# Optimization experiments

Measured on AMD Instinct MI355X. Metric: run time of the kernel, lower is better.

The kernel has to match this reference:

```python
import jax, jax.numpy as jnp
import numpy as np

N_NODES = 50000
N_EDGES = 1600000
E_DIM = 128
N_LAYERS = 3
N_GRAPHS = 32


def setup_inputs() -> dict:
    key = jax.random.key(0)
    ks = jax.random.split(key, 12)
    x = jax.random.normal(ks[0], (N_NODES,), dtype=jnp.float32)
    edge_index = jax.random.randint(ks[1], (2, N_EDGES), 0, N_NODES, dtype=jnp.int32)
    batch = jnp.sort(jax.random.randint(ks[2], (N_NODES,), 0, N_GRAPHS, dtype=jnp.int32))
    s_in = 1.0  # fan_in = 1 for the first linear
    s_e = 1.0 / np.sqrt(E_DIM)
    lin_w = jax.random.normal(ks[3], (1, E_DIM), jnp.float32) * s_in
    lin_b = jax.random.normal(ks[4], (E_DIM,), jnp.float32) * 0.01
    gcn_w = jax.random.normal(ks[5], (N_LAYERS, E_DIM, E_DIM), jnp.float32) * s_e
    gcn_b = jax.random.normal(ks[6], (N_LAYERS, E_DIM), jnp.float32) * 0.01
    r1_w = jax.random.normal(ks[7], (E_DIM, E_DIM), jnp.float32) * s_e
    r1_b = jax.random.normal(ks[8], (E_DIM,), jnp.float32) * 0.01
    r2_w = jax.random.normal(ks[9], (E_DIM, 1), jnp.float32) * s_e
    r2_b = jax.random.normal(ks[10], (1,), jnp.float32) * 0.01
    return {"x": x, "edge_index": edge_index, "batch": batch,
            "lin_w": lin_w, "lin_b": lin_b, "gcn_w": gcn_w, "gcn_b": gcn_b,
            "r1_w": r1_w, "r1_b": r1_b, "r2_w": r2_w, "r2_b": r2_b}


def reference(x, edge_index, batch, lin_w, lin_b, gcn_w, gcn_b, r1_w, r1_b, r2_w, r2_b):
    # input embedding: x.view(-1, 1) @ W + b -> [N, E]
    h = x.reshape(-1, 1) @ lin_w + lin_b

    # GCN normalization (add self-loops, symmetric deg^-1/2 norm) — structure is
    # identical across layers, so compute once.
    loops = jnp.arange(N_NODES, dtype=edge_index.dtype)
    src = jnp.concatenate([edge_index[0], loops])
    dst = jnp.concatenate([edge_index[1], loops])
    deg = jax.ops.segment_sum(jnp.ones(src.shape[0], h.dtype), dst, num_segments=N_NODES)
    dinv = jnp.where(deg > 0, jax.lax.rsqrt(deg), 0.0)
    norm = (dinv[src] * dinv[dst])[:, None]  # [E+N, 1]

    # NOTE: original calls x.relu() without assignment -> no activation (faithful).
    for l in range(N_LAYERS):
        h = h @ gcn_w[l]                                        # [N, E]
        h = jax.ops.segment_sum(h[src] * norm, dst, num_segments=N_NODES) + gcn_b[l]

    # global_add_pool over graphs
    pooled = jax.ops.segment_sum(h, batch, num_segments=N_GRAPHS)  # [G, E]
    hr = jnp.tanh(pooled @ r1_w + r1_b)
    return hr @ r2_w + r2_b  # [G, 1]
```

## Files before the change

### kernel.cpp

```cpp
#include <hip/hip_runtime.h>
#include <math.h>

#define NGRAPH 32
#define CAP 10240
#define EPT 16
#define EPB (256 * EPT)
#define BLK 256

__device__ __forceinline__ int block_scan_excl(int v, int tid, int* wsum, int& total) {
    int x = v;
#pragma unroll
    for (int d = 1; d < 64; d <<= 1) {
        int t = __shfl_up(x, d);
        if ((tid & 63) >= d) x += t;
    }
    if ((tid & 63) == 63) wsum[tid >> 6] = x;
    __syncthreads();
    if (tid == 0) {
        int a = 0;
#pragma unroll
        for (int i = 0; i < 4; i++) { int t = wsum[i]; wsum[i] = a; a += t; }
        wsum[4] = a;
    }
    __syncthreads();
    total = wsum[4];
    return x - v + wsum[tid >> 6];
}

__global__ __launch_bounds__(256, 4) void k_part(
        const int* __restrict__ src, const int* __restrict__ dst,
        int* __restrict__ gcursor, unsigned int* __restrict__ packed, int E) {
    __shared__ unsigned int ldsbuf[EPB];
    __shared__ int hist[256], lofs[256], lcur[256], base[256], wsum[5];
    int tid = threadIdx.x;
    int e0 = blockIdx.x * EPB;
    hist[tid] = 0;
    __syncthreads();
    int d_[EPT], s_[EPT];
#pragma unroll
    for (int c = 0; c < EPT / 4; c++) {
        int e = e0 + c * 1024 + (tid << 2);
        if (e + 3 < E) {
            int4 dv = *(const int4*)&dst[e];
            int4 sv = *(const int4*)&src[e];
            d_[4*c+0] = dv.x; d_[4*c+1] = dv.y; d_[4*c+2] = dv.z; d_[4*c+3] = dv.w;
            s_[4*c+0] = sv.x; s_[4*c+1] = sv.y; s_[4*c+2] = sv.z; s_[4*c+3] = sv.w;
            atomicAdd(&hist[dv.x >> 8], 1);
            atomicAdd(&hist[dv.y >> 8], 1);
            atomicAdd(&hist[dv.z >> 8], 1);
            atomicAdd(&hist[dv.w >> 8], 1);
        } else {
#pragma unroll
            for (int k = 0; k < 4; k++) {
                int ee = e + k;
                if (ee < E) {
                    d_[4*c+k] = dst[ee]; s_[4*c+k] = src[ee];
                    atomicAdd(&hist[d_[4*c+k] >> 8], 1);
                } else {
                    d_[4*c+k] = -1;
                }
            }
        }
    }
    __syncthreads();
    int v = hist[tid];
    int total;
    int excl = block_scan_excl(v, tid, wsum, total);
    lofs[tid] = excl;
    lcur[tid] = excl;
    if (v > 0) base[tid] = tid * CAP + atomicAdd(&gcursor[tid], v);
    __syncthreads();
#pragma unroll
    for (int c = 0; c < EPT; c++) {
        int dd = d_[c];
        if (dd >= 0) {
            int bk = dd >> 8;
            int slot = atomicAdd(&lcur[bk], 1);
            ldsbuf[slot] = ((unsigned int)bk << 24) | ((unsigned int)s_[c] << 8)
                         | (unsigned int)(dd & 255);
        }
    }
    __syncthreads();
    for (int i = tid; i < total; i += BLK) {
        unsigned int w = ldsbuf[i];
        int bk = w >> 24;
        packed[base[bk] + (i - lofs[bk])] = w & 0xFFFFFFu;
    }
}

__global__ __launch_bounds__(256) void k_bucket_chain(
        const unsigned int* __restrict__ packed, const int* __restrict__ gcursor,
        const float* __restrict__ x, const int* __restrict__ batch,
        int* __restrict__ offs, int* __restrict__ deg,
        float* __restrict__ dinv, float2* __restrict__ q0,
        float2* __restrict__ q1, float2* __restrict__ q2,
        unsigned short* __restrict__ csr, float* __restrict__ S, int N, int NB,
        const float* __restrict__ lin_w, const float* __restrict__ lin_b,
        const float* __restrict__ gcn_w, const float* __restrict__ gcn_b,
        float* __restrict__ chainv) {
    __shared__ union {
        struct {
            unsigned int buf[CAP];
            __align__(16) unsigned short lcsr[CAP];
            int cnt[256], lcur[256], wsum[5];
            float cs[NGRAPH];
        } b;
        struct { float v4[512]; } c;
    } sm;
    int tid = threadIdx.x;
    int b = blockIdx.x;

    if (b == NB) {
        float* v4 = sm.c.v4;
        int j = tid & 127, gg = tid >> 7;
        if (tid < 128) {
            v4[tid]       = lin_w[tid];
            v4[128 + tid] = lin_b[tid];
            v4[256 + tid] = gcn_b[tid];
            v4[384 + tid] = gcn_b[128 + tid];
        }
        __syncthreads();
        for (int l = 0; l < 3; l++) {
            const float* W = gcn_w + l * 128 * 128;
            float a0 = 0.f, a1 = 0.f;
            for (int k0 = 0; k0 < 128; k0 += 16) {
                float wreg[16];
#pragma unroll
                for (int t = 0; t < 16; t++) wreg[t] = W[(k0 + t) * 128 + j];
#pragma unroll
                for (int t = 0; t < 16; t++) {
                    a0 += v4[gg * 128 + k0 + t] * wreg[t];
                    a1 += v4[(gg + 2) * 128 + k0 + t] * wreg[t];
                }
            }
            __syncthreads();
            v4[gg * 128 + j] = a0;
            bool upd = (gg == 0) ? (l >= 1) : (l >= 2);
            if (upd) v4[(gg + 2) * 128 + j] = a1;
            __syncthreads();
        }
        chainv[tid]       = v4[tid];
        chainv[256 + tid] = v4[256 + tid];
        return;
    }

    int start = b * CAP;
    int len = gcursor[b];
    sm.b.cnt[tid] = 0;
    if (tid < NGRAPH) sm.b.cs[tid] = 0.f;
    __syncthreads();
    for (int e = tid; e < len; e += BLK) {
        unsigned int w = packed[start + e];
        sm.b.buf[e] = w;
        atomicAdd(&sm.b.cnt[w & 255], 1);
    }
    __syncthreads();
    int v = sm.b.cnt[tid];
    int vp = (v + 7) & ~7;
    int total;
    int excl = block_scan_excl(vp, tid, sm.b.wsum, total);
    sm.b.lcur[tid] = excl;
    int node = b * 256 + tid;
    if (node < N) {
        deg[node] = v;
        offs[node] = start + excl;
        float dv = rsqrtf((float)(v + 1));
        dinv[node] = dv;
        q0[node] = make_float2(x[node] * dv, dv);
        atomicAdd(&sm.b.cs[batch[node]], 1.f);
        for (int p = v; p < vp; p++)
            sm.b.lcsr[excl + p] = (unsigned short)N;
    }
    if (b == 0 && tid == 0) {
        q0[N] = make_float2(0.f, 0.f);
        q1[N] = make_float2(0.f, 0.f);
        q2[N] = make_float2(0.f, 0.f);
    }
    __syncthreads();
    for (int e = tid; e < len; e += BLK) {
        unsigned int w = sm.b.buf[e];
        sm.b.lcsr[atomicAdd(&sm.b.lcur[w & 255], 1)] = (unsigned short)(w >> 8);
    }
    if (tid < NGRAPH && sm.b.cs[tid] != 0.f) atomicAdd(&S[tid], sm.b.cs[tid]);
    __syncthreads();
    const uint4* ls = (const uint4*)sm.b.lcsr;
    uint4* gs = (uint4*)&csr[start];
    for (int i = tid; i < (total >> 3); i += BLK) gs[i] = ls[i];
}

__global__ __launch_bounds__(256) void k_hop1(
        const float2* __restrict__ qin, float2* __restrict__ outv,
        const unsigned short* __restrict__ csr,
        const int* __restrict__ offs, const int* __restrict__ deg,
        const float* __restrict__ dinv, int N) {
    int tid  = threadIdx.x;
    int lane = tid & 3;
    int node = blockIdx.x * 64 + (tid >> 2);
    if (node >= N) return;
    int e = offs[node], ne = deg[node];
    float sx = 0.0f, su = 0.0f;
    for (int j = 8 * lane; j < ne; j += 32) {
        ushort4 c0 = *(const ushort4*)&csr[e + j];
        ushort4 c1 = *(const ushort4*)&csr[e + j + 4];
        float2 a0 = qin[c0.x], a1 = qin[c0.y], a2 = qin[c0.z], a3 = qin[c0.w];
        float2 b0 = qin[c1.x], b1 = qin[c1.y], b2 = qin[c1.z], b3 = qin[c1.w];
        sx += ((a0.x + a1.x) + (a2.x + a3.x)) + ((b0.x + b1.x) + (b2.x + b3.x));
        su += ((a0.y + a1.y) + (a2.y + a3.y)) + ((b0.y + b1.y) + (b2.y + b3.y));
    }
#pragma unroll
    for (int m = 2; m > 0; m >>= 1) {
        sx += __shfl_xor(sx, m);
        su += __shfl_xor(su, m);
    }
    if (lane == 0) {
        float2 qs = qin[node];
        float dv = dinv[node];
        float px = dv * (sx + qs.x), pu = dv * (su + qs.y);
        outv[node] = make_float2(px * dv, pu * dv);
    }
}

__global__ __launch_bounds__(256) void k_hop2(
        const float2* __restrict__ qin, float2* __restrict__ outv,
        const unsigned short* __restrict__ csr,
        const int* __restrict__ offs, const int* __restrict__ deg,
        const float* __restrict__ dinv, const int* __restrict__ batch,
        float* __restrict__ gp1, int N, int NBLK) {
    __shared__ float aS[NGRAPH];
    int tid  = threadIdx.x;
    int lane = tid & 3;
    int node = blockIdx.x * 64 + (tid >> 2);
    if (tid < NGRAPH) aS[tid] = 0.f;
    __syncthreads();
    if (node < N) {
        int e = offs[node], ne = deg[node];
        float sx = 0.0f, su = 0.0f;
        for (int j = 8 * lane; j < ne; j += 32) {
            ushort4 c0 = *(const ushort4*)&csr[e + j];
            ushort4 c1 = *(const ushort4*)&csr[e + j + 4];
            float2 a0 = qin[c0.x], a1 = qin[c0.y], a2 = qin[c0.z], a3 = qin[c0.w];
            float2 b0 = qin[c1.x], b1 = qin[c1.y], b2 = qin[c1.z], b3 = qin[c1.w];
            sx += ((a0.x + a1.x) + (a2.x + a3.x)) + ((b0.x + b1.x) + (b2.x + b3.x));
            su += ((a0.y + a1.y) + (a2.y + a3.y)) + ((b0.y + b1.y) + (b2.y + b3.y));
        }
#pragma unroll
        for (int m = 2; m > 0; m >>= 1) {
            sx += __shfl_xor(sx, m);
            su += __shfl_xor(su, m);
        }
        if (lane == 0) {
            float2 qs = qin[node];
            float dv = dinv[node];
            float px = dv * (sx + qs.x), pu = dv * (su + qs.y);
            outv[node] = make_float2(px * dv, pu * dv);
            atomicAdd(&aS[batch[node]], qs.y * (1.0f / dv));
        }
    }
    __syncthreads();
    if (tid < NGRAPH) gp1[tid * NBLK + blockIdx.x] = aS[tid];
}

__global__ __launch_bounds__(256) void k_hop3(
        const float2* __restrict__ qin,
        const unsigned short* __restrict__ csr,
        const int* __restrict__ offs, const int* __restrict__ deg,
        const float* __restrict__ dinv, const int* __restrict__ batch,
        float* __restrict__ gp2, float* __restrict__ gp3, float* __restrict__ gp4,
        int N, int NBLK) {
    __shared__ float aS[NGRAPH], aV[NGRAPH], aU[NGRAPH];
    int tid  = threadIdx.x;
    int lane = tid & 3;
    int node = blockIdx.x * 64 + (tid >> 2);
    if (tid < NGRAPH) { aS[tid] = 0.f; aV[tid] = 0.f; aU[tid] = 0.f; }
    __syncthreads();
    if (node < N) {
        int e = offs[node], ne = deg[node];
        float sx = 0.0f, su = 0.0f;
        for (int j = 8 * lane; j < ne; j += 32) {
            ushort4 c0 = *(const ushort4*)&csr[e + j];
            ushort4 c1 = *(const ushort4*)&csr[e + j + 4];
            float2 a0 = qin[c0.x], a1 = qin[c0.y], a2 = qin[c0.z], a3 = qin[c0.w];
            float2 b0 = qin[c1.x], b1 = qin[c1.y], b2 = qin[c1.z], b3 = qin[c1.w];
            sx += ((a0.x + a1.x) + (a2.x + a3.x)) + ((b0.x + b1.x) + (b2.x + b3.x));
            su += ((a0.y + a1.y) + (a2.y + a3.y)) + ((b0.y + b1.y) + (b2.y + b3.y));
        }
#pragma unroll
        for (int m = 2; m > 0; m >>= 1) {
            sx += __shfl_xor(sx, m);
            su += __shfl_xor(su, m);
        }
        if (lane == 0) {
            float2 qs = qin[node];
            float dv = dinv[node];
            float px = dv * (sx + qs.x), pu = dv * (su + qs.y);
            int g = batch[node];
            atomicAdd(&aS[g], qs.y * (1.0f / dv));
            atomicAdd(&aV[g], px);
            atomicAdd(&aU[g], pu);
        }
    }
    __syncthreads();
    if (tid < NGRAPH) {
        int slot = tid * NBLK + blockIdx.x;
        gp2[slot] = aS[tid];
        gp3[slot] = aV[tid];
        gp4[slot] = aU[tid];
    }
}

__global__ __launch_bounds__(256) void k_mlp(
        const float* __restrict__ S, const float* __restrict__ chainv,
        const float* __restrict__ gp1, const float* __restrict__ gp2,
        const float* __restrict__ gp3, const float* __restrict__ gp4,
        const float* __restrict__ gcn_b,
        const float* __restrict__ r1_w, const float* __restrict__ r1_b,
        const float* __restrict__ r2_w, const float* __restrict__ r2_b,
        float* __restrict__ out, int NBLK) {
    __shared__ float pl[128], red[128], r4[256];
    int tid = threadIdx.x;
    int g = blockIdx.x;
    float su1 = 0.f, su2 = 0.f, sv3 = 0.f, su3 = 0.f;
    for (int b = tid; b < NBLK; b += BLK) {
        su1 += gp1[g * NBLK + b];
        su2 += gp2[g * NBLK + b];
        sv3 += gp3[g * NBLK + b];
        su3 += gp4[g * NBLK + b];
    }
#pragma unroll
    for (int m = 32; m > 0; m >>= 1) {
        su1 += __shfl_xor(su1, m);
        su2 += __shfl_xor(su2, m);
        su3 += __shfl_xor(su3, m);
        sv3 += __shfl_xor(sv3, m);
    }
    int wv = tid >> 6;
    if ((tid & 63) == 0) {
        r4[wv] = su1; r4[4 + wv] = su2; r4[8 + wv] = su3; r4[12 + wv] = sv3;
    }
    __syncthreads();
    su1 = r4[0] + r4[1] + r4[2] + r4[3];
    su2 = r4[4] + r4[5] + r4[6] + r4[7];
    su3 = r4[8] + r4[9] + r4[10] + r4[11];
    sv3 = r4[12] + r4[13] + r4[14] + r4[15];
    float cnt = S[g];
    const float* b3 = gcn_b + 2 * 128;
    if (tid < 128)
        pl[tid] = sv3 * chainv[tid] + su3 * chainv[128 + tid] + su2 * chainv[256 + tid]
                + su1 * chainv[384 + tid] + cnt * b3[tid];
    __syncthreads();
    int j = tid & 127, half = tid >> 7;
    float acc = 0.f;
#pragma unroll 8
    for (int kk = 0; kk < 64; kk++) {
        int k = half * 64 + kk;
        acc += pl[k] * r1_w[k * 128 + j];
    }
    r4[half * 128 + j] = acc;
    __syncthreads();
    if (tid < 128) {
        float a = r4[tid] + r4[128 + tid] + r1_b[tid];
        red[tid] = tanhf(a) * r2_w[tid];
    }
    __syncthreads();
    for (int sft = 64; sft > 0; sft >>= 1) {
        if (tid < sft) red[tid] += red[tid + sft];
        __syncthreads();
    }
    if (tid == 0) out[g] = red[0] + r2_b[0];
}

extern "C" void kernel_launch(void* const* d_in, const int* in_sizes, int n_in,
                              void* d_out, int out_size, void* d_ws, size_t ws_size,
                              hipStream_t stream) {
    const float* x     = (const float*)d_in[0];
    const int*   eidx  = (const int*)d_in[1];
    const int*   batch = (const int*)d_in[2];
    const float* lin_w = (const float*)d_in[3];
    const float* lin_b = (const float*)d_in[4];
    const float* gcn_w = (const float*)d_in[5];
    const float* gcn_b = (const float*)d_in[6];
    const float* r1_w  = (const float*)d_in[7];
    const float* r1_b  = (const float*)d_in[8];
    const float* r2_w  = (const float*)d_in[9];
    const float* r2_b  = (const float*)d_in[10];

    const int N = in_sizes[0];
    const int E = in_sizes[1] / 2;
    const int* src = eidx;
    const int* dst = eidx + E;
    const int NB = (N + 255) / 256;
    const int hop_blocks = (N + 63) / 64;

    char* w = (char*)d_ws;
    float2* q0      = (float2*)w; w += (size_t)(N + 2) * 8;
    float2* q1      = (float2*)w; w += (size_t)(N + 2) * 8;
    float2* q2      = (float2*)w; w += (size_t)(N + 2) * 8;
    unsigned int* packed = (unsigned int*)w; w += (size_t)256 * CAP * 4;
    int*    offs    = (int*)w;    w += (size_t)N * 4;
    int*    deg     = (int*)w;    w += (size_t)N * 4;
    float*  dinv    = (float*)w;  w += (size_t)N * 4;
    float*  gp1     = (float*)w;  w += (size_t)NGRAPH * hop_blocks * 4;
    float*  gp2     = (float*)w;  w += (size_t)NGRAPH * hop_blocks * 4;
    float*  gp3     = (float*)w;  w += (size_t)NGRAPH * hop_blocks * 4;
    float*  gp4     = (float*)w;  w += (size_t)NGRAPH * hop_blocks * 4;
    int*    gcursor = (int*)w;    w += 256 * 4;
    float*  S       = (float*)w;  w += 64 * 4;
    float*  chainv  = (float*)w;  w += 512 * 4;
    unsigned short* csr = (unsigned short*)w; w += (size_t)256 * CAP * 2 + 256;

    hipMemsetAsync(gcursor, 0, 256 * 4 + 64 * 4, stream);

    const int nchunk = (E + EPB - 1) / EPB;
    k_part<<<nchunk, 256, 0, stream>>>(src, dst, gcursor, packed, E);
    k_bucket_chain<<<NB + 1, 256, 0, stream>>>(packed, gcursor, x, batch, offs, deg,
                                               dinv, q0, q1, q2, csr, S, N, NB,
                                               lin_w, lin_b, gcn_w, gcn_b, chainv);

    k_hop1<<<hop_blocks, 256, 0, stream>>>(q0, q1, csr, offs, deg, dinv, N);
    k_hop2<<<hop_blocks, 256, 0, stream>>>(q1, q2, csr, offs, deg, dinv, batch,
                                           gp1, N, hop_blocks);
    k_hop3<<<hop_blocks, 256, 0, stream>>>(q2, csr, offs, deg, dinv, batch,
                                           gp2, gp3, gp4, N, hop_blocks);

    k_mlp<<<NGRAPH, 256, 0, stream>>>(S, chainv, gp1, gp2, gp3, gp4, gcn_b,
                                      r1_w, r1_b, r2_w, r2_b, (float*)d_out, hop_blocks);
}
```

Measured before the change: 153.0 us.

## Pack offs/deg into int2 meta, recompute dinv, use 8 lanes per node with pad-4

Merges the per-node offset and degree arrays into one int2 meta array and drops the dinv array, recomputing rsqrt and sqrt of (deg+1) in the hop kernels instead. The CSR padding drops from 8 to 4 entries per node, and each hop kernel now gives every node 8 lanes that each gather 4 neighbours per step, instead of 4 lanes gathering 8. This cuts padding waste in the neighbour gathers and the number of metadata loads. In exchange there are fewer gathers in flight per thread, twice as many blocks, and one more shuffle reduction step.

```diff
diff --git a/kernel.cpp b/kernel.cpp
--- a/kernel.cpp
+++ b/kernel.cpp
@@ -91,8 +91,7 @@
 __global__ __launch_bounds__(256) void k_bucket_chain(
         const unsigned int* __restrict__ packed, const int* __restrict__ gcursor,
         const float* __restrict__ x, const int* __restrict__ batch,
-        int* __restrict__ offs, int* __restrict__ deg,
-        float* __restrict__ dinv, float2* __restrict__ q0,
+        int2* __restrict__ meta, float2* __restrict__ q0,
         float2* __restrict__ q1, float2* __restrict__ q2,
         unsigned short* __restrict__ csr, float* __restrict__ S, int N, int NB,
         const float* __restrict__ lin_w, const float* __restrict__ lin_b,
@@ -156,16 +155,14 @@
     }
     __syncthreads();
     int v = sm.b.cnt[tid];
-    int vp = (v + 7) & ~7;
+    int vp = (v + 3) & ~3;
     int total;
     int excl = block_scan_excl(vp, tid, sm.b.wsum, total);
     sm.b.lcur[tid] = excl;
     int node = b * 256 + tid;
     if (node < N) {
-        deg[node] = v;
-        offs[node] = start + excl;
+        meta[node] = make_int2(start + excl, v);
         float dv = rsqrtf((float)(v + 1));
-        dinv[node] = dv;
         q0[node] = make_float2(x[node] * dv, dv);
         atomicAdd(&sm.b.cs[batch[node]], 1.f);
         for (int p = v; p < vp; p++)
@@ -183,38 +180,36 @@
     }
     if (tid < NGRAPH && sm.b.cs[tid] != 0.f) atomicAdd(&S[tid], sm.b.cs[tid]);
     __syncthreads();
-    const uint4* ls = (const uint4*)sm.b.lcsr;
-    uint4* gs = (uint4*)&csr[start];
-    for (int i = tid; i < (total >> 3); i += BLK) gs[i] = ls[i];
+    const uint2* ls = (const uint2*)sm.b.lcsr;
+    uint2* gs = (uint2*)&csr[start];
+    for (int i = tid; i < (total >> 2); i += BLK) gs[i] = ls[i];
 }
 
 __global__ __launch_bounds__(256) void k_hop1(
         const float2* __restrict__ qin, float2* __restrict__ outv,
         const unsigned short* __restrict__ csr,
-        const int* __restrict__ offs, const int* __restrict__ deg,
-        const float* __restrict__ dinv, int N) {
+        const int2* __restrict__ meta, int N) {
     int tid  = threadIdx.x;
-    int lane = tid & 3;
-    int node = blockIdx.x * 64 + (tid >> 2);
+    int lane = tid & 7;
+    int node = blockIdx.x * 32 + (tid >> 3);
     if (node >= N) return;
-    int e = offs[node], ne = deg[node];
+    int2 md = meta[node];
+    int e = md.x, ne = md.y;
     float sx = 0.0f, su = 0.0f;
-    for (int j = 8 * lane; j < ne; j += 32) {
-        ushort4 c0 = *(const ushort4*)&csr[e + j];
-        ushort4 c1 = *(const ushort4*)&csr[e + j + 4];
-        float2 a0 = qin[c0.x], a1 = qin[c0.y], a2 = qin[c0.z], a3 = qin[c0.w];
-        float2 b0 = qin[c1.x], b1 = qin[c1.y], b2 = qin[c1.z], b3 = qin[c1.w];
-        sx += ((a0.x + a1.x) + (a2.x + a3.x)) + ((b0.x + b1.x) + (b2.x + b3.x));
-        su += ((a0.y + a1.y) + (a2.y + a3.y)) + ((b0.y + b1.y) + (b2.y + b3.y));
-    }
-#pragma unroll
-    for (int m = 2; m > 0; m >>= 1) {
+    for (int j = 4 * lane; j < ne; j += 32) {
+        ushort4 c = *(const ushort4*)&csr[e + j];
+        float2 a0 = qin[c.x], a1 = qin[c.y], a2 = qin[c.z], a3 = qin[c.w];
+        sx += (a0.x + a1.x) + (a2.x + a3.x);
+        su += (a0.y + a1.y) + (a2.y + a3.y);
+    }
+#pragma unroll
+    for (int m = 4; m > 0; m >>= 1) {
         sx += __shfl_xor(sx, m);
         su += __shfl_xor(su, m);
     }
     if (lane == 0) {
         float2 qs = qin[node];
-        float dv = dinv[node];
+        float dv = rsqrtf((float)(ne + 1));
         float px = dv * (sx + qs.x), pu = dv * (su + qs.y);
         outv[node] = make_float2(px * dv, pu * dv);
     }
@@ -223,37 +218,35 @@
 __global__ __launch_bounds__(256) void k_hop2(
         const float2* __restrict__ qin, float2* __restrict__ outv,
         const unsigned short* __restrict__ csr,
-        const int* __restrict__ offs, const int* __restrict__ deg,
-        const float* __restrict__ dinv, const int* __restrict__ batch,
+        const int2* __restrict__ meta, const int* __restrict__ batch,
         float* __restrict__ gp1, int N, int NBLK) {
     __shared__ float aS[NGRAPH];
     int tid  = threadIdx.x;
-    int lane = tid & 3;
-    int node = blockIdx.x * 64 + (tid >> 2);
+    int lane = tid & 7;
+    int node = blockIdx.x * 32 + (tid >> 3);
     if (tid < NGRAPH) aS[tid] = 0.f;
     __syncthreads();
     if (node < N) {
-        int e = offs[node], ne = deg[node];
+        int2 md = meta[node];
+        int e = md.x, ne = md.y;
         float sx = 0.0f, su = 0.0f;
-        for (int j = 8 * lane; j < ne; j += 32) {
-            ushort4 c0 = *(const ushort4*)&csr[e + j];
-            ushort4 c1 = *(const ushort4*)&csr[e + j + 4];
-            float2 a0 = qin[c0.x], a1 = qin[c0.y], a2 = qin[c0.z], a3 = qin[c0.w];
-            float2 b0 = qin[c1.x], b1 = qin[c1.y], b2 = qin[c1.z], b3 = qin[c1.w];
-            sx += ((a0.x + a1.x) + (a2.x + a3.x)) + ((b0.x + b1.x) + (b2.x + b3.x));
-            su += ((a0.y + a1.y) + (a2.y + a3.y)) + ((b0.y + b1.y) + (b2.y + b3.y));
-        }
-#pragma unroll
-        for (int m = 2; m > 0; m >>= 1) {
+        for (int j = 4 * lane; j < ne; j += 32) {
+            ushort4 c = *(const ushort4*)&csr[e + j];
+            float2 a0 = qin[c.x], a1 = qin[c.y], a2 = qin[c.z], a3 = qin[c.w];
+            sx += (a0.x + a1.x) + (a2.x + a3.x);
+            su += (a0.y + a1.y) + (a2.y + a3.y);
+        }
+#pragma unroll
+        for (int m = 4; m > 0; m >>= 1) {
             sx += __shfl_xor(sx, m);
             su += __shfl_xor(su, m);
         }
         if (lane == 0) {
             float2 qs = qin[node];
-            float dv = dinv[node];
+            float dv = rsqrtf((float)(ne + 1));
             float px = dv * (sx + qs.x), pu = dv * (su + qs.y);
             outv[node] = make_float2(px * dv, pu * dv);
-            atomicAdd(&aS[batch[node]], qs.y * (1.0f / dv));
+            atomicAdd(&aS[batch[node]], qs.y * sqrtf((float)(ne + 1)));
         }
     }
     __syncthreads();
@@ -263,38 +256,36 @@
 __global__ __launch_bounds__(256) void k_hop3(
         const float2* __restrict__ qin,
         const unsigned short* __restrict__ csr,
-        const int* __restrict__ offs, const int* __restrict__ deg,
-        const float* __restrict__ dinv, const int* __restrict__ batch,
+        const int2* __restrict__ meta, const int* __restrict__ batch,
         float* __restrict__ gp2, float* __restrict__ gp3, float* __restrict__ gp4,
         int N, int NBLK) {
     __shared__ float aS[NGRAPH], aV[NGRAPH], aU[NGRAPH];
     int tid  = threadIdx.x;
-    int lane = tid & 3;
-    int node = blockIdx.x * 64 + (tid >> 2);
+    int lane = tid & 7;
+    int node = blockIdx.x * 32 + (tid >> 3);
     if (tid < NGRAPH) { aS[tid] = 0.f; aV[tid] = 0.f; aU[tid] = 0.f; }
     __syncthreads();
     if (node < N) {
-        int e = offs[node], ne = deg[node];
+        int2 md = meta[node];
+        int e = md.x, ne = md.y;
         float sx = 0.0f, su = 0.0f;
-        for (int j = 8 * lane; j < ne; j += 32) {
-            ushort4 c0 = *(const ushort4*)&csr[e + j];
-            ushort4 c1 = *(const ushort4*)&csr[e + j + 4];
-            float2 a0 = qin[c0.x], a1 = qin[c0.y], a2 = qin[c0.z], a3 = qin[c0.w];
-            float2 b0 = qin[c1.x], b1 = qin[c1.y], b2 = qin[c1.z], b3 = qin[c1.w];
-            sx += ((a0.x + a1.x) + (a2.x + a3.x)) + ((b0.x + b1.x) + (b2.x + b3.x));
-            su += ((a0.y + a1.y) + (a2.y + a3.y)) + ((b0.y + b1.y) + (b2.y + b3.y));
-        }
-#pragma unroll
-        for (int m = 2; m > 0; m >>= 1) {
+        for (int j = 4 * lane; j < ne; j += 32) {
+            ushort4 c = *(const ushort4*)&csr[e + j];
+            float2 a0 = qin[c.x], a1 = qin[c.y], a2 = qin[c.z], a3 = qin[c.w];
+            sx += (a0.x + a1.x) + (a2.x + a3.x);
+            su += (a0.y + a1.y) + (a2.y + a3.y);
+        }
+#pragma unroll
+        for (int m = 4; m > 0; m >>= 1) {
             sx += __shfl_xor(sx, m);
             su += __shfl_xor(su, m);
         }
         if (lane == 0) {
             float2 qs = qin[node];
-            float dv = dinv[node];
+            float dv = rsqrtf((float)(ne + 1));
             float px = dv * (sx + qs.x), pu = dv * (su + qs.y);
             int g = batch[node];
-            atomicAdd(&aS[g], qs.y * (1.0f / dv));
+            atomicAdd(&aS[g], qs.y * sqrtf((float)(ne + 1)));
             atomicAdd(&aV[g], px);
             atomicAdd(&aU[g], pu);
         }
@@ -389,16 +380,14 @@
     const int* src = eidx;
     const int* dst = eidx + E;
     const int NB = (N + 255) / 256;
-    const int hop_blocks = (N + 63) / 64;
+    const int hop_blocks = (N + 31) / 32;
 
     char* w = (char*)d_ws;
     float2* q0      = (float2*)w; w += (size_t)(N + 2) * 8;
     float2* q1      = (float2*)w; w += (size_t)(N + 2) * 8;
     float2* q2      = (float2*)w; w += (size_t)(N + 2) * 8;
+    int2*   meta    = (int2*)w;   w += (size_t)N * 8;
     unsigned int* packed = (unsigned int*)w; w += (size_t)256 * CAP * 4;
-    int*    offs    = (int*)w;    w += (size_t)N * 4;
-    int*    deg     = (int*)w;    w += (size_t)N * 4;
-    float*  dinv    = (float*)w;  w += (size_t)N * 4;
     float*  gp1     = (float*)w;  w += (size_t)NGRAPH * hop_blocks * 4;
     float*  gp2     = (float*)w;  w += (size_t)NGRAPH * hop_blocks * 4;
     float*  gp3     = (float*)w;  w += (size_t)NGRAPH * hop_blocks * 4;
@@ -412,15 +401,14 @@
 
     const int nchunk = (E + EPB - 1) / EPB;
     k_part<<<nchunk, 256, 0, stream>>>(src, dst, gcursor, packed, E);
-    k_bucket_chain<<<NB + 1, 256, 0, stream>>>(packed, gcursor, x, batch, offs, deg,
-                                               dinv, q0, q1, q2, csr, S, N, NB,
+    k_bucket_chain<<<NB + 1, 256, 0, stream>>>(packed, gcursor, x, batch, meta,
+                                               q0, q1, q2, csr, S, N, NB,
                                                lin_w, lin_b, gcn_w, gcn_b, chainv);
 
-    k_hop1<<<hop_blocks, 256, 0, stream>>>(q0, q1, csr, offs, deg, dinv, N);
-    k_hop2<<<hop_blocks, 256, 0, stream>>>(q1, q2, csr, offs, deg, dinv, batch,
-                                           gp1, N, hop_blocks);
-    k_hop3<<<hop_blocks, 256, 0, stream>>>(q2, csr, offs, deg, dinv, batch,
-                                           gp2, gp3, gp4, N, hop_blocks);
+    k_hop1<<<hop_blocks, 256, 0, stream>>>(q0, q1, csr, meta, N);
+    k_hop2<<<hop_blocks, 256, 0, stream>>>(q1, q2, csr, meta, batch, gp1, N, hop_blocks);
+    k_hop3<<<hop_blocks, 256, 0, stream>>>(q2, csr, meta, batch, gp2, gp3, gp4,
+                                           N, hop_blocks);
 
     k_mlp<<<NGRAPH, 256, 0, stream>>>(S, chainv, gp1, gp2, gp3, gp4, gcn_b,
                                       r1_w, r1_b, r2_w, r2_b, (float*)d_out, hop_blocks);
```

Result: faster. 148.5 us (-2.9%).
